# Kernel tuning notes

Measured on AMD Instinct MI355X. Metric: run time of the kernel, lower is better.

The kernel has to match this reference:

```python
import jax, jax.numpy as jnp
import numpy as np

# FP4 (E2M1) format constants from the source module
EXP_BITS = 2
MANT_BITS = 1
EXP_BIAS = 1          # 2**(EXP_BITS-1) - 1
FP4_MAX = 6.0         # (1 + 1/2) * 2**( (2**EXP_BITS - 1) - EXP_BIAS )
GROUP = 128           # w_group_size


def _float_to_fp4(x):
    """Encode float -> 4-bit code (sign|exp|mant) with subnormal support.
    Mirrors _float_to_fp(x, exp_bits=2, mant_bits=1, exp_bias=1)."""
    sign = (x < 0).astype(jnp.int32)
    xa = jnp.abs(x)
    zero = xa == 0
    xs = jnp.where(zero, jnp.float32(1e-8), xa)
    max_exp_field = (1 << EXP_BITS) - 1           # 3
    min_normal_exp = 1 - EXP_BIAS                 # 0
    exp_val = jnp.floor(jnp.log2(xs)).astype(jnp.int32)
    is_sub = exp_val < min_normal_exp
    exp_clamped = jnp.clip(exp_val, min_normal_exp, max_exp_field - EXP_BIAS)
    exp_unbiased = exp_clamped + EXP_BIAS
    ms = 1 << MANT_BITS                           # 2
    mant_normal = jnp.clip(
        jnp.round((xs / jnp.exp2(exp_clamped.astype(jnp.float32)) - 1.0) * ms),
        0, ms - 1).astype(jnp.int32)
    mant_sub = jnp.clip(
        jnp.round(xs / jnp.float32(2.0 ** min_normal_exp) * ms),
        0, ms - 1).astype(jnp.int32)
    exp_field = jnp.where(is_sub, 0, exp_unbiased)
    mant_field = jnp.where(is_sub, mant_sub, mant_normal)
    code = (sign << (EXP_BITS + MANT_BITS)) | (exp_field << MANT_BITS) | mant_field
    return jnp.where(zero, 0, code)


def _fp4_to_float(code):
    """Decode 4-bit code -> float32, with subnormals. Mirrors _fp_to_float."""
    zero = code == 0
    sign = ((code >> (EXP_BITS + MANT_BITS)) & 1).astype(jnp.float32)
    raw_exp = ((code >> MANT_BITS) & ((1 << EXP_BITS) - 1)).astype(jnp.float32)
    mant = (code & ((1 << MANT_BITS) - 1)).astype(jnp.float32)
    value_normal = (1.0 + mant / float(1 << MANT_BITS)) * jnp.exp2(raw_exp - EXP_BIAS)
    value_sub = mant / float(1 << MANT_BITS) * jnp.exp2(jnp.float32(1 - EXP_BIAS))
    v = jnp.where(raw_exp == 0, value_sub, value_normal)
    v = jnp.where(sign == 1, -v, v)
    return jnp.where(zero, jnp.float32(0.0), v)


def quantize_dequantize_weight(w):
    """Group-wise (group=128 along in_features) fp4 quantize-dequantize."""
    O, I = w.shape
    wg = w.reshape(O, I // GROUP, GROUP)
    scale = jnp.max(jnp.abs(wg), axis=-1, keepdims=True) / FP4_MAX
    scale = jnp.maximum(scale, jnp.float32(1e-8))
    code = _float_to_fp4(wg / scale)            # int32 codes in [0, 15]
    deq = _fp4_to_float(code) * scale
    return deq.reshape(O, I)


def setup_inputs() -> dict:
    key = jax.random.key(0)
    k1, k2, k3 = jax.random.split(key, 3)
    x = jax.random.normal(k1, (4, 2048, 4096), dtype=jnp.float32)
    weight = jax.random.normal(k2, (4096, 4096), dtype=jnp.float32) * 0.02
    bias = jax.random.normal(k3, (4096,), dtype=jnp.float32) * 0.01
    return {"x": x, "weight": weight, "bias": bias}


def reference(x, weight, bias):
    # fake-quantize weights to FP4 (E2M1) group-wise, then F.linear
    w_deq = quantize_dequantize_weight(weight)
    return jnp.einsum('bsi,oi->bso', x, w_deq) + bias
```

## Files before the change

kernel.cpp:

```cpp
#include <hip/hip_runtime.h>
#include <stdint.h>

#define M_TOT 8192
#define N_TOT 4096
#define K_TOT 4096
#define NTILE 64

typedef __attribute__((ext_vector_type(8))) short bf16x8;
typedef __attribute__((ext_vector_type(4))) float f32x4;
typedef __attribute__((ext_vector_type(2))) unsigned short u16x2;
typedef __attribute__((ext_vector_type(4))) unsigned short u16x4;

typedef const __attribute__((address_space(1))) void* gas1;
typedef __attribute__((address_space(3))) void* las3;

__device__ __forceinline__ unsigned short bf16_rne(float f) {
    union { float f; unsigned int u; } v; v.f = f;
    unsigned int u = v.u;
    return (unsigned short)((u + 0x7FFFu + ((u >> 16) & 1u)) >> 16);
}

__device__ __forceinline__ float fp4_qdq(float wv, float scale) {
    float a = fabsf(wv) / scale;
    float q;
    if      (a <= 0.25f) q = 0.0f;
    else if (a <  1.0f ) q = 0.5f;
    else if (a <= 1.25f) q = 1.0f;
    else if (a <  2.0f ) q = 1.5f;
    else if (a <= 2.5f ) q = 2.0f;
    else if (a <  4.0f ) q = 3.0f;
    else if (a <= 5.0f ) q = 4.0f;
    else                 q = 6.0f;
    float d = q * scale;
    return wv < 0.0f ? -d : d;
}

__global__ __launch_bounds__(256) void prep_kernel(const float* __restrict__ w,
                                                   unsigned short* __restrict__ wb,
                                                   const float* __restrict__ x,
                                                   unsigned short* __restrict__ xb) {
    if (blockIdx.x < 2048) {
        const int total4 = (M_TOT * K_TOT) / 4;
        int stride = 2048 * 256;
        for (int i = blockIdx.x * 256 + threadIdx.x; i < total4; i += stride) {
            float4 v = ((const float4*)x)[i];
            u16x4 o;
            o.x = bf16_rne(v.x); o.y = bf16_rne(v.y);
            o.z = bf16_rne(v.z); o.w = bf16_rne(v.w);
            ((u16x4*)xb)[i] = o;
        }
    } else {
        int wv0 = (blockIdx.x - 2048) * 4 + (threadIdx.x >> 6);
        int lane = threadIdx.x & 63;
        const int ngroups = (N_TOT * K_TOT) / 128;
        for (int g = wv0; g < ngroups; g += 2048 * 4) {
            size_t base = (size_t)g * 128;
            float2 v = ((const float2*)(w + base))[lane];
            float mx = fmaxf(fabsf(v.x), fabsf(v.y));
            #pragma unroll
            for (int off = 32; off; off >>= 1) mx = fmaxf(mx, __shfl_xor(mx, off));
            float scale = fmaxf(mx / 6.0f, 1e-8f);
            u16x2 o;
            o.x = bf16_rne(fp4_qdq(v.x, scale));
            o.y = bf16_rne(fp4_qdq(v.y, scale));
            *(u16x2*)(wb + base + (size_t)lane * 2) = o;
        }
    }
}


#define BAR()      __builtin_amdgcn_s_barrier()
#define SCHEDB()   __builtin_amdgcn_sched_barrier(0)
#define WAITVM8()  asm volatile("s_waitcnt vmcnt(8)" ::: "memory")
#define WAITVM6()  asm volatile("s_waitcnt vmcnt(6)" ::: "memory")
#define WAITVM0()  asm volatile("s_waitcnt vmcnt(0)" ::: "memory")

__global__ __launch_bounds__(512) void gemm_kernel(const unsigned short* __restrict__ A,
                                                   const unsigned short* __restrict__ B,
                                                   const float* __restrict__ bias,
                                                   float* __restrict__ C) {
    extern __shared__ unsigned char lds[];

    const int bid = blockIdx.x;
    const int xcd = bid & 7;
    const int idx = bid >> 3;
    const int tm = ((xcd >> 2) << 4) + (idx >> 2);
    const int tn = ((xcd & 3) << 2) + (idx & 3);
    const int m0 = tm << 8, n0 = tn << 8;

    const int t = threadIdx.x;
    const int l = t & 63;
    const int wid = t >> 6;
    const int wr = wid >> 2;
    const int wc = wid & 3;
    const int l15 = l & 15;
    const int q4 = l >> 4;

    unsigned offA[8];
    #pragma unroll
    for (int QM = 0; QM < 2; ++QM)
        #pragma unroll
        for (int i = 0; i < 4; ++i) {
            int ra = wr * 128 + QM * 64 + i * 16 + l15;
            unsigned pa = (unsigned)((q4 + (ra >> 1)) & 3);
            offA[QM * 4 + i] = (unsigned)ra * 64u + pa * 16u;
        }
    unsigned offB[4];
    #pragma unroll
    for (int n = 0; n < 4; ++n) {
        int rb = wc * 64 + n * 16 + l15;
        unsigned pb = (unsigned)((q4 + (rb >> 1)) & 3);
        offB[n] = 65536u + (unsigned)rb * 64u + pb * 16u;
    }

    const int r0g = t >> 2,        p0g = t & 3;
    const int r1g = (512 + t) >> 2, p1g = t & 3;
    const int s0g = (p0g - (r0g >> 1)) & 3;
    const int s1g = (p1g - (r1g >> 1)) & 3;
    const unsigned short* arow0 = A + (size_t)(m0 + r0g) * K_TOT + s0g * 8;
    const unsigned short* arow1 = A + (size_t)(m0 + r1g) * K_TOT + s1g * 8;
    const unsigned short* brow0 = B + (size_t)(n0 + r0g) * K_TOT + s0g * 8;
    const unsigned short* brow1 = B + (size_t)(n0 + r1g) * K_TOT + s1g * 8;
    const unsigned lo0 = (unsigned)t * 16u;
    const unsigned lo1 = lo0 + 8192u;

#define STAGE(ROW0, ROW1, MATOFF, KK, TT, BB) do {                                   \
      const unsigned _base = (MATOFF) + (unsigned)(BB) * 32768u + (KK) * 16384u;     \
      const int _ko = (TT) * 64 + (KK) * 32;                                         \
      __builtin_amdgcn_global_load_lds((gas1)(ROW0 + _ko), (las3)(lds + _base + lo0), 16, 0, 0); \
      __builtin_amdgcn_global_load_lds((gas1)(ROW1 + _ko), (las3)(lds + _base + lo1), 16, 0, 0); \
    } while (0)
#define STAGE_A(KK, TT, BB) STAGE(arow0, arow1, 0u, KK, TT, BB)
#define STAGE_B(KK, TT, BB) STAGE(brow0, brow1, 65536u, KK, TT, BB)

#define LOAD_A4(DST, QM, KK, BB) do {                                                \
      _Pragma("unroll")                                                              \
      for (int i = 0; i < 4; ++i)                                                    \
        DST[i] = *(const bf16x8*)(lds + ((BB) * 32768u + (KK) * 16384u)              \
                                  + offA[(QM) * 4 + i]);                             \
    } while (0)

#define LOAD_B4(DST, KK, BB) do {                                                    \
      _Pragma("unroll")                                                              \
      for (int n = 0; n < 4; ++n)                                                    \
        DST[n] = *(const bf16x8*)(lds + ((BB) * 32768u + (KK) * 16384u) + offB[n]);  \
    } while (0)

#define MFMA16(QM, AF, BG) do {                                                      \
      _Pragma("unroll")                                                              \
      for (int i = 0; i < 4; ++i)                                                    \
        _Pragma("unroll")                                                            \
        for (int n = 0; n < 4; ++n)                                                  \
          acc[(QM) * 4 + i][n] = __builtin_amdgcn_mfma_f32_16x16x32_bf16(            \
              AF[i], BG[n], acc[(QM) * 4 + i][n], 0, 0, 0);                          \
    } while (0)

#define KTILE(U, BB) do {                                                            \
      const int tt1 = ((U) + 1 < NTILE) ? (U) + 1 : (U) - 1;                         \
      const int tt2 = ((U) + 2 < NTILE) ? (U) + 2 : (U);                             \
                                                             \
      STAGE_A(1, tt1, 1 - (BB));                                                     \
      __builtin_amdgcn_s_setprio(1); MFMA16(0, af0, bgA);                            \
      __builtin_amdgcn_s_setprio(0);                                                 \
      LOAD_A4(af1, 1, 0, BB);                                                        \
      BAR(); SCHEDB();                                                               \
                                                             \
      STAGE_B(0, tt2, BB);                                                           \
      __builtin_amdgcn_s_setprio(1); MFMA16(1, af1, bgA);                            \
      __builtin_amdgcn_s_setprio(0);                                                 \
      LOAD_B4(bgB, 1, BB); LOAD_A4(af0, 0, 1, BB);                                   \
      BAR(); SCHEDB();                                                               \
                                                             \
      STAGE_A(0, tt2, BB);                                                           \
      __builtin_amdgcn_s_setprio(1); MFMA16(0, af0, bgB);                            \
      __builtin_amdgcn_s_setprio(0);                                                 \
      LOAD_A4(af1, 1, 1, BB);                                                        \
      WAITVM8(); SCHEDB(); BAR(); SCHEDB();                                          \
                                                             \
      STAGE_B(1, tt2, BB);                                                           \
      __builtin_amdgcn_s_setprio(1); MFMA16(1, af1, bgB);                            \
      __builtin_amdgcn_s_setprio(0);                                                 \
      LOAD_B4(bgA, 0, 1 - (BB)); LOAD_A4(af0, 0, 0, 1 - (BB));                       \
      WAITVM6(); SCHEDB(); BAR(); SCHEDB();                                          \
    } while (0)

    f32x4 acc[8][4];
    #pragma unroll
    for (int i = 0; i < 8; ++i)
        #pragma unroll
        for (int j = 0; j < 4; ++j)
            acc[i][j] = (f32x4)0.0f;
    bf16x8 af0[4], af1[4], bgA[4], bgB[4];

    STAGE_A(0, 0, 0); STAGE_B(0, 0, 0); STAGE_A(1, 0, 0); STAGE_B(1, 0, 0);
    STAGE_A(0, 1, 1); STAGE_B(0, 1, 1); STAGE_B(1, 1, 1);
    WAITVM6(); SCHEDB();
    BAR(); SCHEDB();
    LOAD_B4(bgA, 0, 0); LOAD_A4(af0, 0, 0, 0);

    #pragma unroll 1
    for (int u = 0; u < NTILE; u += 2) {
        KTILE(u, 0);
        KTILE(u + 1, 1);
    }
    WAITVM0();

    #pragma unroll
    for (int j = 0; j < 4; ++j) {
        int n = n0 + wc * 64 + j * 16 + l15;
        float bv = bias[n];
        #pragma unroll
        for (int i = 0; i < 8; ++i) {
            int mb = m0 + wr * 128 + i * 16 + (q4 << 2);
            #pragma unroll
            for (int r = 0; r < 4; ++r)
                C[(size_t)(mb + r) * N_TOT + n] = acc[i][j][r] + bv;
        }
    }
}

extern "C" void kernel_launch(void* const* d_in, const int* in_sizes, int n_in,
                              void* d_out, int out_size, void* d_ws, size_t ws_size,
                              hipStream_t stream) {
    const float* x    = (const float*)d_in[0];
    const float* w    = (const float*)d_in[1];
    const float* bias = (const float*)d_in[2];
    float* out = (float*)d_out;

    unsigned short* wb = (unsigned short*)d_ws;
    unsigned short* xb = wb + (size_t)N_TOT * K_TOT;

    prep_kernel<<<4096, 256, 0, stream>>>(w, wb, x, xb);

    hipFuncSetAttribute(reinterpret_cast<const void*>(gemm_kernel),
                        hipFuncAttributeMaxDynamicSharedMemorySize, 131072);
    gemm_kernel<<<512, 512, 131072, stream>>>(xb, wb, bias, out);
}
```

Before: 285.7 us.

## Switch GEMM to 32x32x16 bf16 MFMA with new LDS layout and swizzle

Replaces the 16x16x32 MFMA tiling with 32x32x16 MFMA instructions, so each wave issues fewer, larger matrix ops per K-tile and holds 8 f32x16 accumulators. The LDS staging layout is changed to match: rows become 32-byte half-tiles split by k-subslice, with a new XOR swizzle for reads and global-to-LDS writes. The epilogue is remapped to the 32x32 output register layout. This aims to cut LDS read traffic and instruction overhead per FLOP, at the risk of new bank conflicts or less coalesced epilogue stores.

```diff
diff --git a/kernel.cpp b/kernel.cpp
--- a/kernel.cpp
+++ b/kernel.cpp
@@ -7,7 +7,7 @@
 #define NTILE 64
 
 typedef __attribute__((ext_vector_type(8))) short bf16x8;
-typedef __attribute__((ext_vector_type(4))) float f32x4;
+typedef __attribute__((ext_vector_type(16))) float f32x16;
 typedef __attribute__((ext_vector_type(2))) unsigned short u16x2;
 typedef __attribute__((ext_vector_type(4))) unsigned short u16x4;
 
@@ -93,103 +93,97 @@
     const int wid = t >> 6;
     const int wr = wid >> 2;
     const int wc = wid & 3;
-    const int l15 = l & 15;
-    const int q4 = l >> 4;
-
-    unsigned offA[8];
-    #pragma unroll
-    for (int QM = 0; QM < 2; ++QM)
-        #pragma unroll
-        for (int i = 0; i < 4; ++i) {
-            int ra = wr * 128 + QM * 64 + i * 16 + l15;
-            unsigned pa = (unsigned)((q4 + (ra >> 1)) & 3);
-            offA[QM * 4 + i] = (unsigned)ra * 64u + pa * 16u;
-        }
-    unsigned offB[4];
-    #pragma unroll
-    for (int n = 0; n < 4; ++n) {
-        int rb = wc * 64 + n * 16 + l15;
-        unsigned pb = (unsigned)((q4 + (rb >> 1)) & 3);
-        offB[n] = 65536u + (unsigned)rb * 64u + pb * 16u;
-    }
-
-    const int r0g = t >> 2,        p0g = t & 3;
-    const int r1g = (512 + t) >> 2, p1g = t & 3;
-    const int s0g = (p0g - (r0g >> 1)) & 3;
-    const int s1g = (p1g - (r1g >> 1)) & 3;
-    const unsigned short* arow0 = A + (size_t)(m0 + r0g) * K_TOT + s0g * 8;
-    const unsigned short* arow1 = A + (size_t)(m0 + r1g) * K_TOT + s1g * 8;
-    const unsigned short* brow0 = B + (size_t)(n0 + r0g) * K_TOT + s0g * 8;
-    const unsigned short* brow1 = B + (size_t)(n0 + r1g) * K_TOT + s1g * 8;
+    const int l31 = l & 31;
+    const int h32 = l >> 5;
+
+    const unsigned cread = (unsigned)(h32 ^ ((l31 >> 2) & 1));
+    unsigned offA[4];
+    #pragma unroll
+    for (int mi = 0; mi < 4; ++mi)
+        offA[mi] = (unsigned)(wr * 128 + mi * 32 + l31) * 32u + cread * 16u;
+    unsigned offB[2];
+    #pragma unroll
+    for (int nj = 0; nj < 2; ++nj)
+        offB[nj] = 65536u + (unsigned)(wc * 64 + nj * 32 + l31) * 32u + cread * 16u;
+
+    const int sr = t >> 1;
+    const int scol = ((t & 1) ^ ((t >> 3) & 1)) * 8;
+    const unsigned short* arow = A + (size_t)(m0 + sr) * K_TOT + scol;
+    const unsigned short* brow = B + (size_t)(n0 + sr) * K_TOT + scol;
     const unsigned lo0 = (unsigned)t * 16u;
     const unsigned lo1 = lo0 + 8192u;
 
-#define STAGE(ROW0, ROW1, MATOFF, KK, TT, BB) do {                                   \
+#define STAGE(ROWP, MATOFF, KK, TT, BB) do {                                         \
       const unsigned _base = (MATOFF) + (unsigned)(BB) * 32768u + (KK) * 16384u;     \
       const int _ko = (TT) * 64 + (KK) * 32;                                         \
-      __builtin_amdgcn_global_load_lds((gas1)(ROW0 + _ko), (las3)(lds + _base + lo0), 16, 0, 0); \
-      __builtin_amdgcn_global_load_lds((gas1)(ROW1 + _ko), (las3)(lds + _base + lo1), 16, 0, 0); \
-    } while (0)
-#define STAGE_A(KK, TT, BB) STAGE(arow0, arow1, 0u, KK, TT, BB)
-#define STAGE_B(KK, TT, BB) STAGE(brow0, brow1, 65536u, KK, TT, BB)
-
-#define LOAD_A4(DST, QM, KK, BB) do {                                                \
+      __builtin_amdgcn_global_load_lds((gas1)(ROWP + _ko), (las3)(lds + _base + lo0), 16, 0, 0); \
+      __builtin_amdgcn_global_load_lds((gas1)(ROWP + _ko + 16), (las3)(lds + _base + lo1), 16, 0, 0); \
+    } while (0)
+#define STAGE_A(KK, TT, BB) STAGE(arow, 0u, KK, TT, BB)
+#define STAGE_B(KK, TT, BB) STAGE(brow, 65536u, KK, TT, BB)
+
+#define LOAD_A4(DST, MIH, KK, BB) do {                                               \
       _Pragma("unroll")                                                              \
-      for (int i = 0; i < 4; ++i)                                                    \
-        DST[i] = *(const bf16x8*)(lds + ((BB) * 32768u + (KK) * 16384u)              \
-                                  + offA[(QM) * 4 + i]);                             \
+      for (int i2 = 0; i2 < 2; ++i2)                                                 \
+        _Pragma("unroll")                                                            \
+        for (int ks = 0; ks < 2; ++ks)                                               \
+          DST[i2 * 2 + ks] = *(const bf16x8*)(lds + ((BB) * 32768u + (KK) * 16384u   \
+                               + (unsigned)ks * 8192u) + offA[(MIH) * 2 + i2]);      \
     } while (0)
 
 #define LOAD_B4(DST, KK, BB) do {                                                    \
       _Pragma("unroll")                                                              \
-      for (int n = 0; n < 4; ++n)                                                    \
-        DST[n] = *(const bf16x8*)(lds + ((BB) * 32768u + (KK) * 16384u) + offB[n]);  \
-    } while (0)
-
-#define MFMA16(QM, AF, BG) do {                                                      \
+      for (int nj = 0; nj < 2; ++nj)                                                 \
+        _Pragma("unroll")                                                            \
+        for (int ks = 0; ks < 2; ++ks)                                               \
+          DST[nj * 2 + ks] = *(const bf16x8*)(lds + ((BB) * 32768u + (KK) * 16384u   \
+                               + (unsigned)ks * 8192u) + offB[nj]);                  \
+    } while (0)
+
+#define MFMA8(MIH, AF, BG) do {                                                      \
       _Pragma("unroll")                                                              \
-      for (int i = 0; i < 4; ++i)                                                    \
+      for (int i2 = 0; i2 < 2; ++i2)                                                 \
         _Pragma("unroll")                                                            \
-        for (int n = 0; n < 4; ++n)                                                  \
-          acc[(QM) * 4 + i][n] = __builtin_amdgcn_mfma_f32_16x16x32_bf16(            \
-              AF[i], BG[n], acc[(QM) * 4 + i][n], 0, 0, 0);                          \
+        for (int nj = 0; nj < 2; ++nj)                                               \
+          _Pragma("unroll")                                                          \
+          for (int ks = 0; ks < 2; ++ks)                                             \
+            acc[((MIH) * 2 + i2) * 2 + nj] = __builtin_amdgcn_mfma_f32_32x32x16_bf16( \
+                AF[i2 * 2 + ks], BG[nj * 2 + ks], acc[((MIH) * 2 + i2) * 2 + nj],    \
+                0, 0, 0);                                                            \
     } while (0)
 
 #define KTILE(U, BB) do {                                                            \
       const int tt1 = ((U) + 1 < NTILE) ? (U) + 1 : (U) - 1;                         \
       const int tt2 = ((U) + 2 < NTILE) ? (U) + 2 : (U);                             \
-                                                             \
+                                                         \
       STAGE_A(1, tt1, 1 - (BB));                                                     \
-      __builtin_amdgcn_s_setprio(1); MFMA16(0, af0, bgA);                            \
+      __builtin_amdgcn_s_setprio(1); MFMA8(0, af0, bgA);                             \
       __builtin_amdgcn_s_setprio(0);                                                 \
       LOAD_A4(af1, 1, 0, BB);                                                        \
       BAR(); SCHEDB();                                                               \
-                                                             \
+                                                         \
       STAGE_B(0, tt2, BB);                                                           \
-      __builtin_amdgcn_s_setprio(1); MFMA16(1, af1, bgA);                            \
+      __builtin_amdgcn_s_setprio(1); MFMA8(1, af1, bgA);                             \
       __builtin_amdgcn_s_setprio(0);                                                 \
       LOAD_B4(bgB, 1, BB); LOAD_A4(af0, 0, 1, BB);                                   \
       BAR(); SCHEDB();                                                               \
-                                                             \
+                                                         \
       STAGE_A(0, tt2, BB);                                                           \
-      __builtin_amdgcn_s_setprio(1); MFMA16(0, af0, bgB);                            \
+      __builtin_amdgcn_s_setprio(1); MFMA8(0, af0, bgB);                             \
       __builtin_amdgcn_s_setprio(0);                                                 \
       LOAD_A4(af1, 1, 1, BB);                                                        \
       WAITVM8(); SCHEDB(); BAR(); SCHEDB();                                          \
-                                                             \
+                                                         \
       STAGE_B(1, tt2, BB);                                                           \
-      __builtin_amdgcn_s_setprio(1); MFMA16(1, af1, bgB);                            \
+      __builtin_amdgcn_s_setprio(1); MFMA8(1, af1, bgB);                             \
       __builtin_amdgcn_s_setprio(0);                                                 \
       LOAD_B4(bgA, 0, 1 - (BB)); LOAD_A4(af0, 0, 0, 1 - (BB));                       \
       WAITVM6(); SCHEDB(); BAR(); SCHEDB();                                          \
     } while (0)
 
-    f32x4 acc[8][4];
-    #pragma unroll
-    for (int i = 0; i < 8; ++i)
-        #pragma unroll
-        for (int j = 0; j < 4; ++j)
-            acc[i][j] = (f32x4)0.0f;
+    f32x16 acc[8];
+    #pragma unroll
+    for (int i = 0; i < 8; ++i) acc[i] = (f32x16)0.0f;
     bf16x8 af0[4], af1[4], bgA[4], bgB[4];
 
     STAGE_A(0, 0, 0); STAGE_B(0, 0, 0); STAGE_A(1, 0, 0); STAGE_B(1, 0, 0);
@@ -206,17 +200,18 @@
     WAITVM0();
 
     #pragma unroll
-    for (int j = 0; j < 4; ++j) {
-        int n = n0 + wc * 64 + j * 16 + l15;
-        float bv = bias[n];
+    for (int mi = 0; mi < 4; ++mi)
         #pragma unroll
-        for (int i = 0; i < 8; ++i) {
-            int mb = m0 + wr * 128 + i * 16 + (q4 << 2);
+        for (int nj = 0; nj < 2; ++nj) {
+            int n = n0 + wc * 64 + nj * 32 + l31;
+            float bv = bias[n];
+            int mbase = m0 + wr * 128 + mi * 32 + 4 * h32;
             #pragma unroll
-            for (int r = 0; r < 4; ++r)
-                C[(size_t)(mb + r) * N_TOT + n] = acc[i][j][r] + bv;
+            for (int reg = 0; reg < 16; ++reg) {
+                int row = mbase + (reg & 3) + 8 * (reg >> 2);
+                C[(size_t)row * N_TOT + n] = acc[mi * 2 + nj][reg] + bv;
+            }
         }
-    }
 }
 
 extern "C" void kernel_launch(void* const* d_in, const int* in_sizes, int n_in,
```

Measured after the change: 310.6 us. +8.7%, slower.
